# Kernel tuning notes

Measured on AMD Instinct MI355X. Metric: run time of the kernel, lower is better.

## Reference

```python
import jax, jax.numpy as jnp
import numpy as np

N = 50000       # nodes
E = 1_600_000   # edges (avg degree 32)
IN = 256        # in_dim
HID = 64        # hidden_dim
HEADS = 2
CLS = 10
NEG_SLOPE = 0.2  # PyG GATConv default leaky_relu slope


def gat_layer(x, edge_index, W, att_src, att_dst, bias, heads, concat):
    """PyG-style GATConv (eval mode, add_self_loops=True).
    x: [N, F_in]; W: [F_in, heads*C]; att_src/att_dst: [heads, C]; bias: [heads*C] or [C].
    """
    n = x.shape[0]
    loop = jnp.arange(n)
    src = jnp.concatenate([edge_index[0], loop])   # message sources j
    dst = jnp.concatenate([edge_index[1], loop])   # message targets i
    C = W.shape[1] // heads
    h = (x @ W).reshape(n, heads, C)               # [N, H, C]
    a_s = jnp.sum(h * att_src, axis=-1)            # [N, H]
    a_d = jnp.sum(h * att_dst, axis=-1)            # [N, H]
    e = jax.nn.leaky_relu(a_s[src] + a_d[dst], NEG_SLOPE)   # [E', H]
    # segment softmax over incoming edges of each destination node
    m = jax.lax.stop_gradient(jax.ops.segment_max(e, dst, num_segments=n))
    ex = jnp.exp(e - m[dst])
    denom = jax.ops.segment_sum(ex, dst, num_segments=n)
    alpha = ex / denom[dst]                         # [E', H]
    out = jax.ops.segment_sum(alpha[:, :, None] * h[src], dst, num_segments=n)  # [N, H, C]
    out = out.reshape(n, heads * C) if concat else out.mean(axis=1)
    return out + bias


def setup_inputs() -> dict:
    key = jax.random.key(0)
    ks = jax.random.split(key, 12)
    sd = lambda f: np.float32(1.0 / np.sqrt(f))
    x = jax.random.normal(ks[0], (N, IN), dtype=jnp.float32)
    edge_index = jax.random.randint(ks[1], (2, E), 0, N, dtype=jnp.int64)
    # layer 1: in_dim -> hidden, heads=2, concat
    W1 = jax.random.normal(ks[2], (IN, HEADS * HID), dtype=jnp.float32) * sd(IN)
    as1 = jax.random.normal(ks[3], (HEADS, HID), dtype=jnp.float32) * sd(HID)
    ad1 = jax.random.normal(ks[4], (HEADS, HID), dtype=jnp.float32) * sd(HID)
    b1 = jnp.zeros((HEADS * HID,), dtype=jnp.float32)
    # layer 2: hidden*heads -> hidden, heads=1, concat=False
    W2 = jax.random.normal(ks[5], (HEADS * HID, HID), dtype=jnp.float32) * sd(HEADS * HID)
    as2 = jax.random.normal(ks[6], (1, HID), dtype=jnp.float32) * sd(HID)
    ad2 = jax.random.normal(ks[7], (1, HID), dtype=jnp.float32) * sd(HID)
    b2 = jnp.zeros((HID,), dtype=jnp.float32)
    # linear head
    Wl = jax.random.normal(ks[8], (HID, CLS), dtype=jnp.float32) * sd(HID)
    bl = jnp.zeros((CLS,), dtype=jnp.float32)
    return {"x": x, "edge_index": edge_index,
            "W1": W1, "as1": as1, "ad1": ad1, "b1": b1,
            "W2": W2, "as2": as2, "ad2": ad2, "b2": b2,
            "Wl": Wl, "bl": bl}


def reference(x, edge_index, W1, as1, ad1, b1, W2, as2, ad2, b2, Wl, bl):
    h = jax.nn.elu(gat_layer(x, edge_index, W1, as1, ad1, b1, HEADS, True))
    h = jax.nn.elu(gat_layer(h, edge_index, W2, as2, ad2, b2, 1, False))
    return h @ Wl + bl  # [N, num_classes]
```

## Files before the change

### kernel.cpp

```cpp
#include <hip/hip_runtime.h>

#define NN 50000
#define NE 1600000
#define EP (NE + NN)
#define IN_DIM 256
#define HIDD 64
#define NCLS 10
#define NBKT 196
#define EPB 8192
#define NPB ((EP + EPB - 1) / EPB)
#define BCAP 12288

typedef unsigned short u16;
typedef short bf16x8 __attribute__((ext_vector_type(8)));
typedef float f32x4 __attribute__((ext_vector_type(4)));

__device__ __forceinline__ float b2f(u16 v) { return __uint_as_float(((unsigned)v) << 16); }
__device__ __forceinline__ u16 f2b(float f) {
    unsigned u = __float_as_uint(f);
    unsigned r = (u + 0x7FFFu + ((u >> 16) & 1u)) >> 16;
    return (u16)r;
}

__global__ void detect_mode_k(const int* __restrict__ ei, int* __restrict__ mode,
                              int* __restrict__ gcursor) {
    int t = threadIdx.x;
    for (int i = t; i < NBKT; i += 64) gcursor[i] = 0;
    int nz = 0;
#pragma unroll
    for (int k = 0; k < 4; ++k) {
        int i = t * 4 + k;
        if (ei[2 * i + 1] != 0) nz = 1;
    }
    unsigned long long b = __ballot(nz);
    if (t == 0) *mode = (b == 0ULL) ? 1 : 0;
}

__device__ __forceinline__ void load_edge(const int* __restrict__ ei, int m, int g,
                                          int& s, int& d) {
    if (g < NE) {
        if (m) { s = ei[2 * (size_t)g]; d = ei[2 * ((size_t)NE + g)]; }
        else   { s = ei[g];             d = ei[NE + g]; }
    } else {
        s = d = g - NE;
    }
    s = s < 0 ? 0 : (s >= NN ? NN - 1 : s);
    d = d < 0 ? 0 : (d >= NN ? NN - 1 : d);
}

__global__ __launch_bounds__(256) void wcvt_att_k(
    const float* __restrict__ W, const float* __restrict__ as,
    const float* __restrict__ ad, int K, int N, int H, u16* __restrict__ Wt) {
    int idx = blockIdx.x * 256 + threadIdx.x;
    if (idx >= K * (N + 16)) return;
    int n = idx / K, k = idx - n * K;
    if (n < N) { Wt[idx] = f2b(W[(size_t)k * N + n]); return; }
    int j = n - N;
    if (j >= 2 * H) { Wt[idx] = 0; return; }
    const float* att = (j & 1) ? ad : as;
    int h = j >> 1, C = N / H;
    float sum = 0.f;
    for (int c = 0; c < C; ++c)
        sum += W[(size_t)k * N + h * C + c] * att[h * C + c];
    Wt[idx] = f2b(sum);
}

__global__ __launch_bounds__(256) void partition_k(const int* __restrict__ ei,
                                                   const int* __restrict__ mode,
                                                   int* __restrict__ gcursor,
                                                   unsigned* __restrict__ bbuf) {
    __shared__ int hist[NBKT], base[NBKT], cur[NBKT];
    __shared__ unsigned stash[EPB];
    int t = threadIdx.x;
    for (int i = t; i < NBKT; i += 256) hist[i] = 0;
    __syncthreads();
    int m = *mode;
    int g0 = blockIdx.x * EPB;
    int gend = min(g0 + EPB, EP);
    for (int g = g0 + t; g < gend; g += 256) {
        int s, d;
        load_edge(ei, m, g, s, d);
        stash[g - g0] = ((unsigned)s << 16) | (unsigned)d;
        atomicAdd(&hist[d >> 8], 1);
    }
    __syncthreads();
    for (int i = t; i < NBKT; i += 256) {
        base[i] = hist[i] ? atomicAdd(&gcursor[i], hist[i]) : 0;
        cur[i] = 0;
    }
    __syncthreads();
    int cnt = gend - g0;
    for (int l = t; l < cnt; l += 256) {
        unsigned p = stash[l];
        int d = p & 0xFFFF;
        int b = d >> 8;
        int r = base[b] + atomicAdd(&cur[b], 1);
        if (r < BCAP)
            bbuf[(size_t)b * BCAP + r] = ((p >> 16) << 8) | (unsigned)(d & 255);
    }
}

__global__ __launch_bounds__(256) void bktscan_k(const int* __restrict__ gcursor,
                                                 int* __restrict__ bkt_base) {
    __shared__ int sh[256];
    int t = threadIdx.x;
    int v = (t < NBKT) ? min(gcursor[t], BCAP) : 0;
    sh[t] = v;
    __syncthreads();
    for (int off = 1; off < 256; off <<= 1) {
        int x = (t >= off) ? sh[t - off] : 0;
        __syncthreads();
        sh[t] += x;
        __syncthreads();
    }
    if (t < NBKT) bkt_base[t] = sh[t] - v;
    if (t == NBKT - 1) bkt_base[NBKT] = sh[t];
}

__global__ __launch_bounds__(256) void bucket_csr_k(const unsigned* __restrict__ bbuf,
                                                    const int* __restrict__ gcursor,
                                                    const int* __restrict__ bkt_base,
                                                    int* __restrict__ row_ptr,
                                                    u16* __restrict__ csr_src) {
    __shared__ int hist[256], scan[256], cur[256];
    int b = blockIdx.x, t = threadIdx.x;
    int cnt = min(gcursor[b], BCAP);
    int e0 = bkt_base[b];
    const unsigned* bb = bbuf + (size_t)b * BCAP;
    hist[t] = 0;
    __syncthreads();
    for (int e = t; e < cnt; e += 256)
        atomicAdd(&hist[bb[e] & 255], 1);
    __syncthreads();
    int v = hist[t];
    scan[t] = v;
    __syncthreads();
    for (int off = 1; off < 256; off <<= 1) {
        int x = (t >= off) ? scan[t - off] : 0;
        __syncthreads();
        scan[t] += x;
        __syncthreads();
    }
    int ex = scan[t] - v;
    int n = b * 256 + t;
    if (n < NN) row_ptr[n] = e0 + ex;
    cur[t] = e0 + ex;
    __syncthreads();
    for (int e = t; e < cnt; e += 256) {
        unsigned p = bb[e];
        int pos = atomicAdd(&cur[p & 255], 1);
        csr_src[pos] = (u16)(p >> 8);
    }
    if (b == 0 && t == 0) row_ptr[NN] = bkt_base[NBKT];
}

template <int K, int NF, int H, bool F32A>
__global__ __launch_bounds__(256) void gemm_mfma_att_k(
    const float* __restrict__ Af, const u16* __restrict__ Ab,
    const u16* __restrict__ Wt, u16* __restrict__ C,
    float* __restrict__ a_s, float* __restrict__ a_d) {
    constexpr int NTF = NF / 16, NT = NTF + 1, KS = K / 32;
    const int wave = threadIdx.x >> 6, lane = threadIdx.x & 63;
    const int quad = lane >> 4, l15 = lane & 15;
    const int m0 = blockIdx.x * 64 + wave * 16;
    int rowA = m0 + l15;
    if (rowA >= NN) rowA = NN - 1;
    const float* afp = F32A ? (Af + (size_t)rowA * K + quad * 8) : nullptr;
    const u16*   abp = F32A ? nullptr : (Ab + (size_t)rowA * K + quad * 8);
    const u16* bptr = Wt + (size_t)l15 * K + quad * 8;
    f32x4 acc[NT] = {};
#pragma unroll
    for (int ks = 0; ks < KS; ++ks) {
        bf16x8 af;
        if (F32A) {
            float4 v0 = *(const float4*)(afp + ks * 32);
            float4 v1 = *(const float4*)(afp + ks * 32 + 4);
            af[0] = (short)f2b(v0.x); af[1] = (short)f2b(v0.y);
            af[2] = (short)f2b(v0.z); af[3] = (short)f2b(v0.w);
            af[4] = (short)f2b(v1.x); af[5] = (short)f2b(v1.y);
            af[6] = (short)f2b(v1.z); af[7] = (short)f2b(v1.w);
        } else {
            af = *(const bf16x8*)(abp + ks * 32);
        }
        bf16x8 bf[NT];
#pragma unroll
        for (int nt = 0; nt < NT; ++nt)
            bf[nt] = *(const bf16x8*)(bptr + (size_t)nt * 16 * K + ks * 32);
#pragma unroll
        for (int nt = 0; nt < NT; ++nt)
            acc[nt] = __builtin_amdgcn_mfma_f32_16x16x32_bf16(af, bf[nt], acc[nt], 0, 0, 0);
    }
#pragma unroll
    for (int nt = 0; nt < NTF; ++nt) {
#pragma unroll
        for (int reg = 0; reg < 4; ++reg) {
            int row = m0 + quad * 4 + reg;
            if (row < NN) C[(size_t)row * NF + nt * 16 + l15] = f2b(acc[nt][reg]);
        }
    }
    if (l15 < 2 * H) {
        int h = l15 >> 1;
        float* dst = (l15 & 1) ? a_d : a_s;
#pragma unroll
        for (int reg = 0; reg < 4; ++reg) {
            int row = m0 + quad * 4 + reg;
            if (row < NN) dst[row * H + h] = acc[NTF][reg];
        }
    }
}

template <int CH, int H, bool HEAD>
__global__ __launch_bounds__(256) void gat_gather_k(
    const int* __restrict__ row_ptr, const u16* __restrict__ csr_src,
    const float* __restrict__ a_s, const float* __restrict__ a_d,
    const u16* __restrict__ h, const float* __restrict__ bias,
    u16* __restrict__ outg, const float* __restrict__ Wl,
    const float* __restrict__ bl, float* __restrict__ outh) {
    constexpr int VEC = CH / 64;
    constexpr int JB = 8;
    int n = (blockIdx.x * blockDim.x + threadIdx.x) >> 6;
    int lane = threadIdx.x & 63;
    if (n >= NN) return;
    int r0 = row_ptr[n], r1 = row_ptr[n + 1];
    const bool hi = (VEC == 2) ? (lane >= 32) : false;
    const u16* hlane = h + lane * VEC;

    float adn[H];
#pragma unroll
    for (int hh = 0; hh < H; ++hh) adn[hh] = a_d[n * H + hh];

    float dh0 = 0.f, dh1 = 0.f;
    float acc[VEC];
#pragma unroll
    for (int v = 0; v < VEC; ++v) acc[v] = 0.f;

    for (int base = r0; base < r1; base += 64) {
        int cnt = min(64, r1 - base);
        int idx = base + lane;
        bool act = idx < r1;
        int sl = act ? (int)csr_src[idx] : 0;
        float exl0 = 0.f, exl1 = 0.f;
        {
            float e = a_s[sl * H + 0] + adn[0];
            e = e > 0.f ? e : 0.2f * e;
            e = fminf(e, 60.f);
            exl0 = act ? __expf(e) : 0.f;
            dh0 += exl0;
        }
        if (H == 2) {
            float e = a_s[sl * H + 1] + adn[1];
            e = e > 0.f ? e : 0.2f * e;
            e = fminf(e, 60.f);
            exl1 = act ? __expf(e) : 0.f;
            dh1 += exl1;
        }
        for (int j0 = 0; j0 < cnt; j0 += JB) {
            int ss[JB];
            float exv[JB];
#pragma unroll
            for (int i = 0; i < JB; ++i) {
                int j = j0 + i;
                ss[i] = __shfl(sl, j);
                if (H == 1) {
                    exv[i] = __shfl(exl0, j);
                } else {
                    float e0 = __shfl(exl0, j);
                    float e1 = __shfl(exl1, j);
                    exv[i] = hi ? e1 : e0;
                }
            }
            if (VEC == 2) {
                unsigned hv[JB];
#pragma unroll
                for (int i = 0; i < JB; ++i)
                    hv[i] = *(const unsigned*)(hlane + (size_t)ss[i] * CH);
#pragma unroll
                for (int i = 0; i < JB; ++i) {
                    float lo = __uint_as_float(hv[i] << 16);
                    float hv1 = __uint_as_float(hv[i] & 0xFFFF0000u);
                    acc[0] += exv[i] * lo;
                    acc[1] += exv[i] * hv1;
                }
            } else {
                u16 hv[JB];
#pragma unroll
                for (int i = 0; i < JB; ++i)
                    hv[i] = hlane[(size_t)ss[i] * CH];
#pragma unroll
                for (int i = 0; i < JB; ++i)
                    acc[0] += exv[i] * b2f(hv[i]);
            }
        }
    }

#pragma unroll
    for (int off = 32; off; off >>= 1) dh0 += __shfl_xor(dh0, off);
    float dn = dh0;
    if (H == 2) {
#pragma unroll
        for (int off = 32; off; off >>= 1) dh1 += __shfl_xor(dh1, off);
        dn = hi ? dh1 : dh0;
    }

    if (VEC == 2) {
        int c = lane * 2;
        float2 bv = *(const float2*)(bias + c);
        float v0 = acc[0] / dn + bv.x;
        float v1 = acc[1] / dn + bv.y;
        v0 = v0 > 0.f ? v0 : expm1f(v0);
        v1 = v1 > 0.f ? v1 : expm1f(v1);
        ushort2 ov;
        ov.x = f2b(v0); ov.y = f2b(v1);
        *(ushort2*)(outg + (size_t)n * CH + c) = ov;
    } else {
        float v0 = acc[0] / dn + bias[lane];
        v0 = v0 > 0.f ? v0 : expm1f(v0);
        if (HEAD) {
#pragma unroll
            for (int cls = 0; cls < NCLS; ++cls) {
                float p = v0 * Wl[lane * NCLS + cls];
#pragma unroll
                for (int off = 32; off; off >>= 1) p += __shfl_xor(p, off);
                if (lane == cls) outh[(size_t)n * NCLS + cls] = p + bl[cls];
            }
        } else {
            outg[(size_t)n * CH + lane] = f2b(v0);
        }
    }
}

extern "C" void kernel_launch(void* const* d_in, const int* in_sizes, int n_in,
                              void* d_out, int out_size, void* d_ws, size_t ws_size,
                              hipStream_t stream) {
    const float* x   = (const float*)d_in[0];
    const int*   ei  = (const int*)d_in[1];
    const float* W1  = (const float*)d_in[2];
    const float* as1 = (const float*)d_in[3];
    const float* ad1 = (const float*)d_in[4];
    const float* b1  = (const float*)d_in[5];
    const float* W2  = (const float*)d_in[6];
    const float* as2 = (const float*)d_in[7];
    const float* ad2 = (const float*)d_in[8];
    const float* b2  = (const float*)d_in[9];
    const float* Wl  = (const float*)d_in[10];
    const float* bl  = (const float*)d_in[11];
    float* out = (float*)d_out;

    float* ws = (float*)d_ws;
    size_t o = 0;
    u16* hb  = (u16*)(ws + o); o += (size_t)NN * 64;
    u16* g1  = (u16*)(ws + o); o += (size_t)NN * 64;
    unsigned* bbuf = (unsigned*)g1;
    u16* w1t = (u16*)(ws + o); o += 144 * 256 / 2;
    u16* w2t = (u16*)(ws + o); o += 80 * 128 / 2;
    float* a_s = ws + o;       o += (size_t)NN * 2;
    float* a_d = ws + o;       o += (size_t)NN * 2;
    int* ints = (int*)(ws + o);
    size_t io = 0;
    int* gcursor  = ints + io; io += NBKT;
    int* bkt_base = ints + io; io += NBKT + 1;
    int* row_ptr  = ints + io; io += NN + 1;
    u16* csr_src  = (u16*)(ints + io); io += (EP + 1) / 2;
    int* mode     = ints + io; io += 1;

    detect_mode_k<<<1, 64, 0, stream>>>(ei, mode, gcursor);

    wcvt_att_k<<<(256 * 144 + 255) / 256, 256, 0, stream>>>(W1, as1, ad1, 256, 128, 2, w1t);
    wcvt_att_k<<<(128 * 80 + 255) / 256, 256, 0, stream>>>(W2, as2, ad2, 128, 64, 1, w2t);

    partition_k<<<NPB, 256, 0, stream>>>(ei, mode, gcursor, bbuf);
    bktscan_k<<<1, 256, 0, stream>>>(gcursor, bkt_base);
    bucket_csr_k<<<NBKT, 256, 0, stream>>>(bbuf, gcursor, bkt_base, row_ptr, csr_src);

    const int gatherBlocks = (NN + 3) / 4;
    const int gemmBlocks = (NN + 63) / 64;

    gemm_mfma_att_k<256, 128, 2, true><<<gemmBlocks, 256, 0, stream>>>(
        x, nullptr, w1t, hb, a_s, a_d);
    gat_gather_k<128, 2, false><<<gatherBlocks, 256, 0, stream>>>(
        row_ptr, csr_src, a_s, a_d, hb, b1, g1, nullptr, nullptr, nullptr);

    gemm_mfma_att_k<128, 64, 1, false><<<gemmBlocks, 256, 0, stream>>>(
        nullptr, g1, w2t, hb, a_s, a_d);
    gat_gather_k<64, 1, true><<<gatherBlocks, 256, 0, stream>>>(
        row_ptr, csr_src, a_s, a_d, hb, b2, nullptr, Wl, bl, out);
}
```

Measured before the change: 371.7 us.

## Merge setup kernels, fold bucket scan into CSR build, pack gather shuffles

Folds mode detection and both weight conversions into one setup kernel, and moves the bucket prefix scan into each bucket_csr block, removing three launches and the bkt_base buffer. In the gather kernel, edge weights are packed as bf16 pairs (or source index plus weight for one head), so fewer shuffles are issued per edge, and a_s/a_d are read as float2. Exp weights are now rounded to bf16 before accumulation, which lowers precision slightly, and every bucket block redundantly recomputes the 196-entry scan.

New measurement: 324.6 us. 1.15x faster.

```diff
diff --git a/kernel.cpp b/kernel.cpp
--- a/kernel.cpp
+++ b/kernel.cpp
@@ -22,20 +22,6 @@
     return (u16)r;
 }
 
-__global__ void detect_mode_k(const int* __restrict__ ei, int* __restrict__ mode,
-                              int* __restrict__ gcursor) {
-    int t = threadIdx.x;
-    for (int i = t; i < NBKT; i += 64) gcursor[i] = 0;
-    int nz = 0;
-#pragma unroll
-    for (int k = 0; k < 4; ++k) {
-        int i = t * 4 + k;
-        if (ei[2 * i + 1] != 0) nz = 1;
-    }
-    unsigned long long b = __ballot(nz);
-    if (t == 0) *mode = (b == 0ULL) ? 1 : 0;
-}
-
 __device__ __forceinline__ void load_edge(const int* __restrict__ ei, int m, int g,
                                           int& s, int& d) {
     if (g < NE) {
@@ -48,10 +34,10 @@
     d = d < 0 ? 0 : (d >= NN ? NN - 1 : d);
 }
 
-__global__ __launch_bounds__(256) void wcvt_att_k(
+__device__ __forceinline__ void wcvt_att_job(
     const float* __restrict__ W, const float* __restrict__ as,
-    const float* __restrict__ ad, int K, int N, int H, u16* __restrict__ Wt) {
-    int idx = blockIdx.x * 256 + threadIdx.x;
+    const float* __restrict__ ad, int K, int N, int H, u16* __restrict__ Wt,
+    int idx) {
     if (idx >= K * (N + 16)) return;
     int n = idx / K, k = idx - n * K;
     if (n < N) { Wt[idx] = f2b(W[(size_t)k * N + n]); return; }
@@ -65,6 +51,32 @@
     Wt[idx] = f2b(sum);
 }
 
+__global__ __launch_bounds__(256) void setup_k(
+    const int* __restrict__ ei, int* __restrict__ mode, int* __restrict__ gcursor,
+    const float* __restrict__ W1, const float* __restrict__ as1,
+    const float* __restrict__ ad1, u16* __restrict__ w1t,
+    const float* __restrict__ W2, const float* __restrict__ as2,
+    const float* __restrict__ ad2, u16* __restrict__ w2t) {
+    int b = blockIdx.x, t = threadIdx.x;
+    if (b == 0) {
+        for (int i = t; i < NBKT; i += 256) gcursor[i] = 0;
+        if (t < 64) {
+            int nz = 0;
+#pragma unroll
+            for (int k = 0; k < 4; ++k) {
+                int i = t * 4 + k;
+                if (ei[2 * i + 1] != 0) nz = 1;
+            }
+            unsigned long long bal = __ballot(nz);
+            if (t == 0) *mode = (bal == 0ULL) ? 1 : 0;
+        }
+    } else if (b <= 144) {
+        wcvt_att_job(W1, as1, ad1, 256, 128, 2, w1t, (b - 1) * 256 + t);
+    } else {
+        wcvt_att_job(W2, as2, ad2, 128, 64, 1, w2t, (b - 145) * 256 + t);
+    }
+}
+
 __global__ __launch_bounds__(256) void partition_k(const int* __restrict__ ei,
                                                    const int* __restrict__ mode,
                                                    int* __restrict__ gcursor,
@@ -100,48 +112,42 @@
     }
 }
 
-__global__ __launch_bounds__(256) void bktscan_k(const int* __restrict__ gcursor,
-                                                 int* __restrict__ bkt_base) {
-    __shared__ int sh[256];
-    int t = threadIdx.x;
-    int v = (t < NBKT) ? min(gcursor[t], BCAP) : 0;
-    sh[t] = v;
-    __syncthreads();
-    for (int off = 1; off < 256; off <<= 1) {
-        int x = (t >= off) ? sh[t - off] : 0;
-        __syncthreads();
-        sh[t] += x;
-        __syncthreads();
-    }
-    if (t < NBKT) bkt_base[t] = sh[t] - v;
-    if (t == NBKT - 1) bkt_base[NBKT] = sh[t];
-}
-
 __global__ __launch_bounds__(256) void bucket_csr_k(const unsigned* __restrict__ bbuf,
                                                     const int* __restrict__ gcursor,
-                                                    const int* __restrict__ bkt_base,
                                                     int* __restrict__ row_ptr,
                                                     u16* __restrict__ csr_src) {
-    __shared__ int hist[256], scan[256], cur[256];
+    __shared__ int bsc[256];
+    __shared__ int hist[256], scn[256], cur[256];
+    __shared__ int se0, scnt, stot;
     int b = blockIdx.x, t = threadIdx.x;
-    int cnt = min(gcursor[b], BCAP);
-    int e0 = bkt_base[b];
+    int v = (t < NBKT) ? min(gcursor[t], BCAP) : 0;
+    bsc[t] = v;
+    __syncthreads();
+    for (int off = 1; off < 256; off <<= 1) {
+        int x = (t >= off) ? bsc[t - off] : 0;
+        __syncthreads();
+        bsc[t] += x;
+        __syncthreads();
+    }
+    if (t == b) { se0 = bsc[t] - v; scnt = v; }
+    if (t == NBKT - 1) stot = bsc[t];
+    hist[t] = 0;
+    __syncthreads();
+    int e0 = se0, cnt = scnt;
     const unsigned* bb = bbuf + (size_t)b * BCAP;
-    hist[t] = 0;
-    __syncthreads();
     for (int e = t; e < cnt; e += 256)
         atomicAdd(&hist[bb[e] & 255], 1);
     __syncthreads();
-    int v = hist[t];
-    scan[t] = v;
+    int hv = hist[t];
+    scn[t] = hv;
     __syncthreads();
     for (int off = 1; off < 256; off <<= 1) {
-        int x = (t >= off) ? scan[t - off] : 0;
+        int x = (t >= off) ? scn[t - off] : 0;
         __syncthreads();
-        scan[t] += x;
+        scn[t] += x;
         __syncthreads();
     }
-    int ex = scan[t] - v;
+    int ex = scn[t] - hv;
     int n = b * 256 + t;
     if (n < NN) row_ptr[n] = e0 + ex;
     cur[t] = e0 + ex;
@@ -151,7 +157,7 @@
         int pos = atomicAdd(&cur[p & 255], 1);
         csr_src[pos] = (u16)(p >> 8);
     }
-    if (b == 0 && t == 0) row_ptr[NN] = bkt_base[NBKT];
+    if (b == 0 && t == 0) row_ptr[NN] = stot;
 }
 
 template <int K, int NF, int H, bool F32A>
@@ -225,9 +231,13 @@
     const bool hi = (VEC == 2) ? (lane >= 32) : false;
     const u16* hlane = h + lane * VEC;
 
-    float adn[H];
-#pragma unroll
-    for (int hh = 0; hh < H; ++hh) adn[hh] = a_d[n * H + hh];
+    float adn0, adn1 = 0.f;
+    if (H == 2) {
+        float2 adv = *(const float2*)(a_d + n * 2);
+        adn0 = adv.x; adn1 = adv.y;
+    } else {
+        adn0 = a_d[n];
+    }
 
     float dh0 = 0.f, dh1 = 0.f;
     float acc[VEC];
@@ -239,56 +249,61 @@
         int idx = base + lane;
         bool act = idx < r1;
         int sl = act ? (int)csr_src[idx] : 0;
-        float exl0 = 0.f, exl1 = 0.f;
-        {
-            float e = a_s[sl * H + 0] + adn[0];
-            e = e > 0.f ? e : 0.2f * e;
-            e = fminf(e, 60.f);
-            exl0 = act ? __expf(e) : 0.f;
-            dh0 += exl0;
-        }
+        unsigned pex;
         if (H == 2) {
-            float e = a_s[sl * H + 1] + adn[1];
-            e = e > 0.f ? e : 0.2f * e;
-            e = fminf(e, 60.f);
-            exl1 = act ? __expf(e) : 0.f;
-            dh1 += exl1;
+            float2 av = *(const float2*)(a_s + sl * 2);
+            float e0 = av.x + adn0;
+            e0 = e0 > 0.f ? e0 : 0.2f * e0;
+            e0 = fminf(e0, 60.f);
+            float ex0 = act ? __expf(e0) : 0.f;
+            dh0 += ex0;
+            float e1 = av.y + adn1;
+            e1 = e1 > 0.f ? e1 : 0.2f * e1;
+            e1 = fminf(e1, 60.f);
+            float ex1 = act ? __expf(e1) : 0.f;
+            dh1 += ex1;
+            pex = (unsigned)f2b(ex0) | ((unsigned)f2b(ex1) << 16);
+        } else {
+            float e0 = a_s[sl] + adn0;
+            e0 = e0 > 0.f ? e0 : 0.2f * e0;
+            e0 = fminf(e0, 60.f);
+            float ex0 = act ? __expf(e0) : 0.f;
+            dh0 += ex0;
+            pex = (unsigned)sl | ((unsigned)f2b(ex0) << 16);
         }
         for (int j0 = 0; j0 < cnt; j0 += JB) {
-            int ss[JB];
-            float exv[JB];
-#pragma unroll
-            for (int i = 0; i < JB; ++i) {
-                int j = j0 + i;
-                ss[i] = __shfl(sl, j);
-                if (H == 1) {
-                    exv[i] = __shfl(exl0, j);
-                } else {
-                    float e0 = __shfl(exl0, j);
-                    float e1 = __shfl(exl1, j);
-                    exv[i] = hi ? e1 : e0;
+            if (VEC == 2) {
+                int ss[JB];
+                unsigned pe[JB];
+#pragma unroll
+                for (int i = 0; i < JB; ++i) {
+                    int j = j0 + i;
+                    ss[i] = __shfl(sl, j);
+                    pe[i] = (unsigned)__shfl((int)pex, j);
                 }
-            }
-            if (VEC == 2) {
                 unsigned hv[JB];
 #pragma unroll
                 for (int i = 0; i < JB; ++i)
                     hv[i] = *(const unsigned*)(hlane + (size_t)ss[i] * CH);
 #pragma unroll
                 for (int i = 0; i < JB; ++i) {
-                    float lo = __uint_as_float(hv[i] << 16);
-                    float hv1 = __uint_as_float(hv[i] & 0xFFFF0000u);
-                    acc[0] += exv[i] * lo;
-                    acc[1] += exv[i] * hv1;
+                    float exv = hi ? __uint_as_float(pe[i] & 0xFFFF0000u)
+                                   : __uint_as_float(pe[i] << 16);
+                    acc[0] += exv * __uint_as_float(hv[i] << 16);
+                    acc[1] += exv * __uint_as_float(hv[i] & 0xFFFF0000u);
                 }
             } else {
+                unsigned pe[JB];
+#pragma unroll
+                for (int i = 0; i < JB; ++i)
+                    pe[i] = (unsigned)__shfl((int)pex, j0 + i);
                 u16 hv[JB];
 #pragma unroll
                 for (int i = 0; i < JB; ++i)
-                    hv[i] = hlane[(size_t)ss[i] * CH];
+                    hv[i] = hlane[(size_t)(pe[i] & 0xFFFFu) * CH];
 #pragma unroll
                 for (int i = 0; i < JB; ++i)
-                    acc[0] += exv[i] * b2f(hv[i]);
+                    acc[0] += __uint_as_float(pe[i] & 0xFFFF0000u) * b2f(hv[i]);
             }
         }
     }
@@ -358,19 +373,15 @@
     int* ints = (int*)(ws + o);
     size_t io = 0;
     int* gcursor  = ints + io; io += NBKT;
-    int* bkt_base = ints + io; io += NBKT + 1;
     int* row_ptr  = ints + io; io += NN + 1;
     u16* csr_src  = (u16*)(ints + io); io += (EP + 1) / 2;
     int* mode     = ints + io; io += 1;
 
-    detect_mode_k<<<1, 64, 0, stream>>>(ei, mode, gcursor);
-
-    wcvt_att_k<<<(256 * 144 + 255) / 256, 256, 0, stream>>>(W1, as1, ad1, 256, 128, 2, w1t);
-    wcvt_att_k<<<(128 * 80 + 255) / 256, 256, 0, stream>>>(W2, as2, ad2, 128, 64, 1, w2t);
+    setup_k<<<185, 256, 0, stream>>>(ei, mode, gcursor,
+                                     W1, as1, ad1, w1t, W2, as2, ad2, w2t);
 
     partition_k<<<NPB, 256, 0, stream>>>(ei, mode, gcursor, bbuf);
-    bktscan_k<<<1, 256, 0, stream>>>(gcursor, bkt_base);
-    bucket_csr_k<<<NBKT, 256, 0, stream>>>(bbuf, gcursor, bkt_base, row_ptr, csr_src);
+    bucket_csr_k<<<NBKT, 256, 0, stream>>>(bbuf, gcursor, row_ptr, csr_src);
 
     const int gatherBlocks = (NN + 3) / 4;
     const int gemmBlocks = (NN + 63) / 64;
```
